# Performance work log

Hardware: AMD Instinct MI355X
Metric: run time of the kernel (lower is better)

Reference implementation:

```python
import jax, jax.numpy as jnp
import numpy as np
from jax import lax

NP = 27  # num_param, perfect cube
N3 = 3   # cube root
EPS = 1e-5


def _conv3d(x, w, stride, pad):
    return lax.conv_general_dilated(
        x, w, window_strides=(stride,) * 3, padding=[(pad, pad)] * 3,
        dimension_numbers=("NCDHW", "OIDHW", "NCDHW"))


def _p_n():
    # torch.meshgrid(arange(3),arange(3),arange(3), indexing='xy') == np.meshgrid 'xy'
    g0, g1, g2 = np.meshgrid(np.arange(N3), np.arange(N3), np.arange(N3), indexing="xy")
    p_n = np.concatenate([g0.ravel(), g1.ravel(), g2.ravel()], 0)  # (3N,)
    return jnp.asarray(p_n, jnp.float32).reshape(1, 3 * NP, 1, 1, 1)


def _p_0(h, w, d):
    # faithful to original: 'xy' meshgrid, flatten, then view(1,1,h,w,d)
    g0, g1, g2 = np.meshgrid(np.arange(h), np.arange(w), np.arange(d), indexing="xy")
    outs = []
    for g in (g0, g1, g2):
        gg = jnp.asarray(g.ravel(), jnp.float32).reshape(1, 1, h, w, d)
        outs.append(jnp.broadcast_to(gg, (1, NP, h, w, d)))
    return jnp.concatenate(outs, axis=1)  # (1, 3N, h, w, d)


def _gather_xq(x_flat, ix, iy, iz, W, D, shape):
    # x_flat: (b, c, H*W*D); i*: (b, h, w, d, N) int32
    idx = ix * (W * D) + iy * D + iz
    b = idx.shape[0]
    idx = jnp.clip(idx, 0, x_flat.shape[-1] - 1).reshape(b, -1)
    xq = jax.vmap(lambda xf, ii: xf[:, ii])(x_flat, idx)  # (b, c, h*w*d*N)
    return xq.reshape(shape)


def reference(x, p_w, p_b, conv_w, gamma, beta):
    b, c, H, W, D = x.shape
    # offset prediction (weight is zero-initialized in original; bias drives offsets)
    offset = _conv3d(x, p_w, 1, 1) + p_b[None, :, None, None, None]  # (b, 3N, h, w, d)
    h, w, d = offset.shape[2:]

    p = _p_0(h, w, d) + _p_n() + offset                 # (b, 3N, h, w, d)
    p = jnp.transpose(p, (0, 2, 3, 4, 1))               # (b, h, w, d, 3N)
    px, py, pz = p[..., :NP], p[..., NP:2 * NP], p[..., 2 * NP:]

    fx, fy, fz = jnp.floor(px), jnp.floor(py), jnp.floor(pz)
    ltx = jnp.clip(fx, 0, H - 1); lty = jnp.clip(fy, 0, W - 1); ltz = jnp.clip(fz, 0, D - 1)
    rbx = jnp.clip(fx + 1, 0, H - 1); rby = jnp.clip(fy + 1, 0, W - 1); rbz = jnp.clip(fz + 1, 0, D - 1)

    pcx = jnp.clip(px, 0, H - 1); pcy = jnp.clip(py, 0, W - 1); pcz = jnp.clip(pz, 0, D - 1)

    # trilinear-style weights (6 corners as in the original)
    g_lt = (1 + (ltx - pcx)) * (1 + (lty - pcy)) * (1 + (ltz - pcz))
    g_rb = (1 - (rbx - pcx)) * (1 - (rby - pcy)) * (1 - (rbz - pcz))
    g_lb = (1 + (ltx - pcx)) * (1 - (rby - pcy)) * (1 + (ltz - pcz))
    g_rt = (1 - (rbx - pcx)) * (1 + (lty - pcy)) * (1 + (ltz - pcz))
    g_lf = (1 + (ltx - pcx)) * (1 + (lty - pcy)) * (1 - (rbz - pcz))
    g_rf = (1 - (rbx - pcx)) * (1 - (rby - pcy)) * (1 + (ltz - pcz))

    i = lambda t: t.astype(jnp.int32)
    x_flat = x.reshape(b, c, -1)
    shp = (b, c, h, w, d, NP)
    xq_lt = _gather_xq(x_flat, i(ltx), i(lty), i(ltz), W, D, shp)
    xq_rb = _gather_xq(x_flat, i(rbx), i(rby), i(rbz), W, D, shp)
    xq_lb = _gather_xq(x_flat, i(ltx), i(rby), i(ltz), W, D, shp)
    xq_rt = _gather_xq(x_flat, i(rbx), i(lty), i(ltz), W, D, shp)
    xq_lf = _gather_xq(x_flat, i(ltx), i(lty), i(rbz), W, D, shp)
    xq_rf = _gather_xq(x_flat, i(rbx), i(rby), i(ltz), W, D, shp)

    e = lambda g: g[:, None]  # (b,1,h,w,d,N)
    x_off = (e(g_lt) * xq_lt + e(g_rb) * xq_rb + e(g_lb) * xq_lb +
             e(g_rt) * xq_rt + e(g_lf) * xq_lf + e(g_rf) * xq_rf)

    # regroup (b,c,h,w,d,27) -> (b,c,3h,3w,3d)
    x_off = x_off.reshape(b, c, h, w, d, N3, N3, N3)
    x_off = jnp.transpose(x_off, (0, 1, 2, 5, 3, 6, 4, 7)).reshape(b, c, h * N3, w * N3, d * N3)

    # Conv3d(stride 2, pad 1, no bias) + BatchNorm3d (train mode, batch stats) + SiLU
    o = _conv3d(x_off, conv_w, 2, 1)
    mean = jnp.mean(o, axis=(0, 2, 3, 4), keepdims=True)
    var = jnp.var(o, axis=(0, 2, 3, 4), keepdims=True)
    y = gamma[None, :, None, None, None] * (o - mean) * lax.rsqrt(var + EPS) + beta[None, :, None, None, None]
    return y * jax.nn.sigmoid(y)


def setup_inputs() -> dict:
    key = jax.random.key(0)
    k1, k2, k3 = jax.random.split(key, 3)
    B, Cin, Cout, S = 2, 16, 32, 32
    x = jax.random.normal(k1, (B, Cin, S, S, S), jnp.float32)
    p_w = jnp.zeros((3 * NP, Cin, 3, 3, 3), jnp.float32)  # zero-init as in original
    bound = 1.0 / np.sqrt(Cin * 27)
    p_b = jax.random.uniform(k2, (3 * NP,), jnp.float32, -bound, bound)
    conv_w = jax.random.normal(k3, (Cout, Cin, 3, 3, 3), jnp.float32) * 0.05
    gamma = jnp.ones((Cout,), jnp.float32)
    beta = jnp.zeros((Cout,), jnp.float32)
    return {"x": x, "p_w": p_w, "p_b": p_b, "conv_w": conv_w, "gamma": gamma, "beta": beta}
```

## Files before the change

### kernel.cpp

```cpp
#include <hip/hip_runtime.h>
#include <hip/hip_bf16.h>

constexpr int BATCH = 2;
constexpr int CIN   = 16;
constexpr int COUT  = 32;
constexpr int HWD   = 32768;
constexpr int BIG   = 96;
constexpr int OUTD  = 48;
constexpr int OUT2  = OUTD * OUTD;
constexpr int OUTN  = OUTD * OUTD * OUTD;
constexpr int NOUT  = BATCH * COUT * OUTN;
constexpr int NBLK3 = 1728;

typedef __attribute__((ext_vector_type(2)))  float f32x2;
typedef __attribute__((ext_vector_type(8)))  short bf16x8;
typedef __attribute__((ext_vector_type(16))) float f32x16;

__device__ __forceinline__ float bf_lo(uint u) { return __uint_as_float(u << 16); }
__device__ __forceinline__ float bf_hi(uint u) { return __uint_as_float(u & 0xFFFF0000u); }
__device__ __forceinline__ f32x2 up2(uint u) {
    f32x2 r; r.x = bf_lo(u); r.y = bf_hi(u); return r;
}

__global__ __launch_bounds__(256) void k_prep(const float* __restrict__ cw,
                                              const float* __restrict__ pw,
                                              const float* __restrict__ x,
                                              ushort* __restrict__ wTb,
                                              ushort* __restrict__ pwTb,
                                              ushort* __restrict__ xb,
                                              uint* __restrict__ lut) {
    int blk = blockIdx.x;
    if (blk < 216) {
        int t = blk * 256 + threadIdx.x;
        if (t < 13824) {
            int ci = t & 15; int rr = t >> 4; int co = rr & 31; int tap = rr >> 5;
            __hip_bfloat16 h = __float2bfloat16(cw[co * 432 + ci * 27 + tap]);
            wTb[t] = *(ushort*)&h;
        } else {
            int u = t - 13824;
            int ci = u & 15; int rr = u >> 4; int oc = rr % 96; int tap = rr / 96;
            float v = (oc < 81) ? pw[oc * 432 + ci * 27 + tap] : 0.f;
            __hip_bfloat16 h = __float2bfloat16(v);
            pwTb[u] = *(ushort*)&h;
        }
    } else if (blk < 222) {
        int e = (blk - 216) * 256 + threadIdx.x;
        if (e < 1445) {
            int su = e / 289; int rm = e - su * 289;
            int sv = rm / 17; int ts = rm - sv * 17;
            int sw = (ts < 9) ? (2 * ts) : (2 * ts - 17);
            lut[e] = (uint)su | ((uint)sv << 8) | ((uint)sw << 16) | ((uint)ts << 24);
        }
    } else {
        int t = (blk - 222) * 256 + threadIdx.x;
        int bt = t >> 15, pos = t & 32767;
        float v[16];
#pragma unroll
        for (int ci = 0; ci < 16; ci++) v[ci] = x[(bt * 16 + ci) * HWD + pos];
        uint uw[8];
#pragma unroll
        for (int cc = 0; cc < 8; cc++) {
            __hip_bfloat16 h0 = __float2bfloat16(v[2 * cc]);
            __hip_bfloat16 h1 = __float2bfloat16(v[2 * cc + 1]);
            uw[cc] = (uint)(*(ushort*)&h0) | ((uint)(*(ushort*)&h1) << 16);
        }
        uint4* xd = (uint4*)(xb + (size_t)t * 16);
        xd[0] = make_uint4(uw[0], uw[1], uw[2], uw[3]);
        xd[1] = make_uint4(uw[4], uw[5], uw[6], uw[7]);
    }
}

__global__ __launch_bounds__(256) void k_offset_mfma(const ushort* __restrict__ xb,
                                                     const ushort* __restrict__ pwTb,
                                                     const float* __restrict__ p_b,
                                                     ushort* __restrict__ offP) {
    __shared__ uint4 repbuf[1728];
    uint4*  lds = repbuf;
    ushort* rep = (ushort*)repbuf;

    int blk = blockIdx.x;
    int bt = blk >> 8; int r = blk & 255;
    int ut = r >> 4; int vt = (r >> 2) & 3; int wt = r & 3;
    int a0 = ut * 2, b0 = vt * 8, c0 = wt * 8;
    int tid = threadIdx.x;
    int wv = tid >> 6, l = tid & 63, col = l & 31, half = l >> 5;

    const ushort* xbb = xb + (size_t)bt * HWD * 16;
    for (int s = tid; s < 800; s += 256) {
        int h = s & 1, p = s >> 1;
        int su = p / 100; int rm = p - su * 100;
        int sv = rm / 10; int sw = rm - sv * 10;
        int ga = a0 - 1 + su, gb = b0 - 1 + sv, gc = c0 - 1 + sw;
        uint4 v = make_uint4(0, 0, 0, 0);
        if ((unsigned)ga < 32u && (unsigned)gb < 32u && (unsigned)gc < 32u)
            v = *(const uint4*)(xbb + (size_t)(ga * 1024 + gb * 32 + gc) * 16 + h * 8);
        lds[((su * 10 + sv) * 11 + sw) * 2 + h] = v;
    }
    __syncthreads();

    int U = wv >> 1, V = ((wv & 1) << 2) + (col >> 3), W = col & 7;
    const uint4* wt4 = (const uint4*)pwTb;

    f32x16 acc[3];
#pragma unroll 1
    for (int g = 0; g < 3; g++) {
        bf16x8 wf[27];
#pragma unroll
        for (int t = 0; t < 27; t++)
            wf[t] = __builtin_bit_cast(bf16x8, wt4[(t * 96 + g * 32 + col) * 2 + half]);
#pragma unroll
        for (int i = 0; i < 16; i++) acc[g][i] = 0.f;
#pragma unroll
        for (int k1 = 0; k1 < 3; k1++)
#pragma unroll
        for (int k2 = 0; k2 < 3; k2++)
#pragma unroll
        for (int k3 = 0; k3 < 3; k3++) {
            bf16x8 xf = __builtin_bit_cast(bf16x8,
                lds[(((U + k1) * 10 + (V + k2)) * 11 + (W + k3)) * 2 + half]);
            acc[g] = __builtin_amdgcn_mfma_f32_32x32x16_bf16(wf[(k1 * 3 + k2) * 3 + k3],
                                                             xf, acc[g], 0, 0, 0);
        }
    }
    __syncthreads();

    int posl = (U * 8 + V) * 8 + W;
#pragma unroll 1
    for (int g = 0; g < 3; g++) {
#pragma unroll
        for (int rg = 0; rg < 16; rg++) {
            int co = g * 32 + (rg & 3) + 8 * (rg >> 2) + 4 * half;
            if (co < 81) {
                int n = co % 27, d = co / 27;
                __hip_bfloat16 h = __float2bfloat16(acc[g][rg] + p_b[co]);
                rep[posl * 108 + n * 4 + d] = *(ushort*)&h;
            }
        }
    }
    __syncthreads();

    const uint* rp = (const uint*)rep;
    uint* og = (uint*)offP + (size_t)bt * HWD * 54;
    for (int f = tid; f < 6912; f += 256) {
        int pl = f / 54; int i = f - pl * 54;
        int pu = pl >> 6, pv = (pl >> 3) & 7, pw2 = pl & 7;
        int pos = (a0 + pu) * 1024 + (b0 + pv) * 32 + (c0 + pw2);
        og[(size_t)pos * 54 + i] = rp[f];
    }
}

__global__ __launch_bounds__(256, 3) void k_fused(const ushort* __restrict__ xb,
                                                  const ushort* __restrict__ offP,
                                                  const ushort* __restrict__ wTb,
                                                  const uint* __restrict__ lut,
                                                  ushort* __restrict__ o16,
                                                  float* __restrict__ psum,
                                                  float* __restrict__ psq) {
    __shared__ uint4 halo[5 * 17 * 19 * 2];
    __shared__ float ls[4][32], lq[4][32];

    int blk = (blockIdx.x & 7) * 216 + (blockIdx.x >> 3);

    int bt = blk / 864; int r = blk - bt * 864;
    int ut = r / 36; r -= ut * 36;
    int vt = r / 6;  int wt = r - vt * 6;

    int tid = threadIdx.x;
    int wv = tid >> 6, l = tid & 63;
    int col = l & 31, half = l >> 5;

    int gU0 = ut * 4 - 1, gV0 = vt * 16 - 1, gW0 = wt * 16 - 1;
    const ushort* xbb  = xb + (size_t)bt * HWD * 16;
    const ushort* offb = offP + (size_t)bt * HWD * 108;

    for (int s = tid; s < 1445; s += 256) {
        uint code = lut[s];
        int su = code & 255, sv = (code >> 8) & 255;
        int sw = (code >> 16) & 255, ts = code >> 24;
        int gU = gU0 + su, gV = gV0 + sv, gW = gW0 + sw;
        float vf = ((gU | gV | gW) >= 0) ? 1.f : 0.f;
        unsigned uU = (unsigned)max(gU, 0);
        unsigned uV = (unsigned)max(gV, 0);
        unsigned uW = (unsigned)max(gW, 0);
        int a = uU / 3u, i = uU - 3u * a;
        int b = uV / 3u, j = uV - 3u * b;
        int c = uW / 3u, kk = uW - 3u * c;
        int n = i * 9 + j * 3 + kk;
        int pos = a * 1024 + b * 32 + c;
        uint2 ou = *(const uint2*)(offb + (size_t)pos * 108 + n * 4);
        float ox = bf_lo(ou.x), oy = bf_hi(ou.x), oz = bf_lo(ou.y);

        float px = (float)(b + j) + ox;
        float py = (float)(a + i) + oy;
        float pz = (float)(c + kk) + oz;

        float fx = floorf(px), fy = floorf(py), fz = floorf(pz);
        float ltx = fminf(fmaxf(fx, 0.f), 31.f);
        float lty = fminf(fmaxf(fy, 0.f), 31.f);
        float ltz = fminf(fmaxf(fz, 0.f), 31.f);
        float rbx = fminf(fmaxf(fx + 1.f, 0.f), 31.f);
        float rby = fminf(fmaxf(fy + 1.f, 0.f), 31.f);
        float rbz = fminf(fmaxf(fz + 1.f, 0.f), 31.f);
        float pcx = fminf(fmaxf(px, 0.f), 31.f);
        float pcy = fminf(fmaxf(py, 0.f), 31.f);
        float pcz = fminf(fmaxf(pz, 0.f), 31.f);

        float axl = (1.f + (ltx - pcx)) * vf, axr = (1.f - (rbx - pcx)) * vf;
        float ayl = 1.f + (lty - pcy), ayr = 1.f - (rby - pcy);
        float azl = 1.f + (ltz - pcz), azr = 1.f - (rbz - pcz);

        float g_lt = axl * ayl * azl;
        float g_rb = axr * ayr * azr;
        float g_lb = axl * ayr * azl;
        float g_rt = axr * ayl * azl;
        float g_lf = axl * ayl * azr;
        float g_rf = axr * ayr * azl;

        int iltx = (int)ltx, ilty = (int)lty, iltz = (int)ltz;
        int irbx = (int)rbx, irby = (int)rby, irbz = (int)rbz;

        int i_lt = iltx * 1024 + ilty * 32 + iltz;
        int i_rb = irbx * 1024 + irby * 32 + irbz;
        int i_lb = iltx * 1024 + irby * 32 + iltz;
        int i_rt = irbx * 1024 + ilty * 32 + iltz;
        int i_lf = iltx * 1024 + ilty * 32 + irbz;
        int i_rf = irbx * 1024 + irby * 32 + iltz;

        f32x2 acc2[8];
#pragma unroll
        for (int q = 0; q < 8; q++) acc2[q] = (f32x2){0.f, 0.f};

        auto corner = [&](float g, int ip) {
            const uint4* p = (const uint4*)(xbb + (size_t)ip * 16);
            uint4 u0 = p[0], u1 = p[1];
            f32x2 g2 = {g, g};
            acc2[0] += g2 * up2(u0.x); acc2[1] += g2 * up2(u0.y);
            acc2[2] += g2 * up2(u0.z); acc2[3] += g2 * up2(u0.w);
            acc2[4] += g2 * up2(u1.x); acc2[5] += g2 * up2(u1.y);
            acc2[6] += g2 * up2(u1.z); acc2[7] += g2 * up2(u1.w);
        };
        corner(g_lt, i_lt);
        corner(g_rb, i_rb);
        corner(g_lb, i_lb);
        corner(g_rt, i_rt);
        corner(g_lf, i_lf);
        corner(g_rf, i_rf);

        uint uw[8];
#pragma unroll
        for (int cc = 0; cc < 8; cc++) {
            __hip_bfloat16 h0 = __float2bfloat16(acc2[cc].x);
            __hip_bfloat16 h1 = __float2bfloat16(acc2[cc].y);
            uw[cc] = (uint)(*(ushort*)&h0) | ((uint)(*(ushort*)&h1) << 16);
        }
        halo[((su * 17 + sv) * 19 + ts) * 2 + 0] = make_uint4(uw[0], uw[1], uw[2], uw[3]);
        halo[((su * 17 + sv) * 19 + ts) * 2 + 1] = make_uint4(uw[4], uw[5], uw[6], uw[7]);
    }

    bf16x8 wf[27];
    const uint4* wt4 = (const uint4*)wTb;
#pragma unroll
    for (int t = 0; t < 27; t++)
        wf[t] = __builtin_bit_cast(bf16x8, wt4[(t * 32 + col) * 2 + half]);

    __syncthreads();

    int U = wv >> 1, V = (wv & 1) * 4 + (col >> 3), W = col & 7;
    const uint4* lp = &halo[(((2 * U * 17 + 2 * V) * 19) + W) * 2 + half];

    f32x16 acc;
#pragma unroll
    for (int i = 0; i < 16; i++) acc[i] = 0.f;

#pragma unroll
    for (int k1 = 0; k1 < 3; k1++)
#pragma unroll
    for (int k2 = 0; k2 < 3; k2++)
#pragma unroll
    for (int k3 = 0; k3 < 3; k3++) {
        const int so = (k3 == 0) ? 0 : (k3 == 1 ? 9 : 1);
        const int off2 = ((k1 * 17 + k2) * 19 + so) * 2;
        bf16x8 xf = __builtin_bit_cast(bf16x8, lp[off2]);
        acc = __builtin_amdgcn_mfma_f32_32x32x16_bf16(wf[(k1 * 3 + k2) * 3 + k3],
                                                      xf, acc, 0, 0, 0);
    }

    int u = ut * 2 + U, v = vt * 8 + V, wg = wt * 8 + W;
    size_t posg = (size_t)u * OUT2 + v * OUTD + wg;
    ushort* ob = o16 + (size_t)bt * COUT * OUTN;
#pragma unroll
    for (int rg = 0; rg < 16; rg++) {
        int co = (rg & 3) + 8 * (rg >> 2) + 4 * half;
        __hip_bfloat16 h = __float2bfloat16(acc[rg]);
        ob[(size_t)co * OUTN + posg] = *(ushort*)&h;
    }

#pragma unroll
    for (int rg = 0; rg < 16; rg++) {
        float s = acc[rg], q = acc[rg] * acc[rg];
#pragma unroll
        for (int o = 1; o < 32; o <<= 1) {
            s += __shfl_xor(s, o);
            q += __shfl_xor(q, o);
        }
        if (col == 0) {
            int co = (rg & 3) + 8 * (rg >> 2) + 4 * half;
            ls[wv][co] = s; lq[wv][co] = q;
        }
    }
    __syncthreads();
    if (tid < 32) {
        float s = ls[0][tid] + ls[1][tid] + ls[2][tid] + ls[3][tid];
        float q = lq[0][tid] + lq[1][tid] + lq[2][tid] + lq[3][tid];
        psum[blk * 32 + tid] = s;
        psq[blk * 32 + tid]  = q;
    }
}

__global__ __launch_bounds__(256) void k_stats(const float* __restrict__ psum,
                                               const float* __restrict__ psq,
                                               const float* __restrict__ gamma,
                                               const float* __restrict__ beta,
                                               float* __restrict__ stats) {
    int co  = blockIdx.x;
    int tid = threadIdx.x;
    float s = 0.f, q = 0.f;
    for (int i = tid; i < NBLK3; i += 256) {
        s += psum[i * 32 + co];
        q += psq[i * 32 + co];
    }
    __shared__ float ss[256], sq[256];
    ss[tid] = s; sq[tid] = q;
    __syncthreads();
    for (int st = 128; st > 0; st >>= 1) {
        if (tid < st) { ss[tid] += ss[tid + st]; sq[tid] += sq[tid + st]; }
        __syncthreads();
    }
    if (tid == 0) {
        const float N = 221184.f;
        float mean = ss[0] / N;
        float var  = sq[0] / N - mean * mean;
        float inv  = rsqrtf(var + 1e-5f);
        float A = gamma[co] * inv;
        stats[co * 2]     = A;
        stats[co * 2 + 1] = beta[co] - A * mean;
    }
}

__global__ __launch_bounds__(256) void k_bn_silu(const ushort* __restrict__ o16,
                                                 const float* __restrict__ stats,
                                                 float* __restrict__ out) {
    int t = blockIdx.x * 256 + threadIdx.x;
    int co = (t / (OUTN / 8)) & 31;
    float A = stats[co * 2], B = stats[co * 2 + 1];
    uint4 u = ((const uint4*)o16)[t];
    float o[8] = {bf_lo(u.x), bf_hi(u.x), bf_lo(u.y), bf_hi(u.y),
                  bf_lo(u.z), bf_hi(u.z), bf_lo(u.w), bf_hi(u.w)};
    float y[8];
#pragma unroll
    for (int q = 0; q < 8; q++) {
        float yy = A * o[q] + B;
        y[q] = yy / (1.f + __expf(-yy));
    }
    float4* dst = (float4*)(out + (size_t)t * 8);
    dst[0] = make_float4(y[0], y[1], y[2], y[3]);
    dst[1] = make_float4(y[4], y[5], y[6], y[7]);
}

extern "C" void kernel_launch(void* const* d_in, const int* in_sizes, int n_in,
                              void* d_out, int out_size, void* d_ws, size_t ws_size,
                              hipStream_t stream) {
    const float* x      = (const float*)d_in[0];
    const float* p_w    = (const float*)d_in[1];
    const float* p_b    = (const float*)d_in[2];
    const float* conv_w = (const float*)d_in[3];
    const float* gamma  = (const float*)d_in[4];
    const float* beta   = (const float*)d_in[5];
    float* out = (float*)d_out;
    float* ws  = (float*)d_ws;

    float* psum  = ws;
    float* psq   = psum + 55296;
    float* stats = psq + 55296;
    ushort* wTb  = (ushort*)(stats + 64);
    ushort* pwTb = wTb + 13824;
    ushort* xb   = pwTb + 41472;
    ushort* offP = xb + 1048576;
    ushort* o16  = offP + 7077888;
    uint*   lut  = (uint*)(o16 + 7077888);

    k_prep<<<478, 256, 0, stream>>>(conv_w, p_w, x, wTb, pwTb, xb, lut);
    k_offset_mfma<<<512, 256, 0, stream>>>(xb, pwTb, p_b, offP);
    k_fused<<<NBLK3, 256, 0, stream>>>(xb, offP, wTb, lut, o16, psum, psq);
    k_stats<<<32, 256, 0, stream>>>(psum, psq, gamma, beta, stats);
    k_bn_silu<<<NOUT / 2048, 256, 0, stream>>>(o16, stats, out);
}
```

Baseline: 107.0 us.

## Use 512-thread blocks for halo gather and keep MFMA on 256 threads

Doubles the k_fused block to 512 threads. All threads share the deformable trilinear gather that fills the shared-memory halo, in a fixed three-iteration unrolled loop. The LUT is padded with dummy entries, written to a spare halo column, so no bounds check is needed. The halo is split into separate low and high channel arrays, and only the first 256 threads load weights and run the MFMA convolution and stats reduction. This aims to hide gather latency with more waves, but leaves half the threads idle during the MFMA phase, and the tighter launch bounds may force register spills of the 27 weight fragments.

```diff
diff --git a/kernel.cpp b/kernel.cpp
--- a/kernel.cpp
+++ b/kernel.cpp
@@ -45,12 +45,15 @@
         }
     } else if (blk < 222) {
         int e = (blk - 216) * 256 + threadIdx.x;
+        uint su, sv, sw, ts;
         if (e < 1445) {
-            int su = e / 289; int rm = e - su * 289;
-            int sv = rm / 17; int ts = rm - sv * 17;
-            int sw = (ts < 9) ? (2 * ts) : (2 * ts - 17);
-            lut[e] = (uint)su | ((uint)sv << 8) | ((uint)sw << 16) | ((uint)ts << 24);
-        }
+            su = e / 289; int rm = e - su * 289;
+            sv = rm / 17; ts = rm - sv * 17;
+            sw = (ts < 9) ? (2 * ts) : (2 * ts - 17);
+        } else {
+            su = 0; sv = (e - 1445) % 17; sw = 0; ts = 17;
+        }
+        lut[e] = su | (sv << 8) | (sw << 16) | (ts << 24);
     } else {
         int t = (blk - 222) * 256 + threadIdx.x;
         int bt = t >> 15, pos = t & 32767;
@@ -149,14 +152,15 @@
     }
 }
 
-__global__ __launch_bounds__(256, 3) void k_fused(const ushort* __restrict__ xb,
+__global__ __launch_bounds__(512, 6) void k_fused(const ushort* __restrict__ xb,
                                                   const ushort* __restrict__ offP,
                                                   const ushort* __restrict__ wTb,
                                                   const uint* __restrict__ lut,
                                                   ushort* __restrict__ o16,
                                                   float* __restrict__ psum,
                                                   float* __restrict__ psq) {
-    __shared__ uint4 halo[5 * 17 * 19 * 2];
+    __shared__ uint4 halo_lo[5 * 17 * 19];
+    __shared__ uint4 halo_hi[5 * 17 * 19];
     __shared__ float ls[4][32], lq[4][32];
 
     int blk = (blockIdx.x & 7) * 216 + (blockIdx.x >> 3);
@@ -166,14 +170,14 @@
     int vt = r / 6;  int wt = r - vt * 6;
 
     int tid = threadIdx.x;
-    int wv = tid >> 6, l = tid & 63;
-    int col = l & 31, half = l >> 5;
 
     int gU0 = ut * 4 - 1, gV0 = vt * 16 - 1, gW0 = wt * 16 - 1;
     const ushort* xbb  = xb + (size_t)bt * HWD * 16;
     const ushort* offb = offP + (size_t)bt * HWD * 108;
 
-    for (int s = tid; s < 1445; s += 256) {
+#pragma unroll
+    for (int it = 0; it < 3; it++) {
+        int s = tid + it * 512;
         uint code = lut[s];
         int su = code & 255, sv = (code >> 8) & 255;
         int sw = (code >> 16) & 255, ts = code >> 24;
@@ -253,59 +257,65 @@
             __hip_bfloat16 h1 = __float2bfloat16(acc2[cc].y);
             uw[cc] = (uint)(*(ushort*)&h0) | ((uint)(*(ushort*)&h1) << 16);
         }
-        halo[((su * 17 + sv) * 19 + ts) * 2 + 0] = make_uint4(uw[0], uw[1], uw[2], uw[3]);
-        halo[((su * 17 + sv) * 19 + ts) * 2 + 1] = make_uint4(uw[4], uw[5], uw[6], uw[7]);
-    }
-
-    bf16x8 wf[27];
-    const uint4* wt4 = (const uint4*)wTb;
-#pragma unroll
-    for (int t = 0; t < 27; t++)
-        wf[t] = __builtin_bit_cast(bf16x8, wt4[(t * 32 + col) * 2 + half]);
-
-    __syncthreads();
-
-    int U = wv >> 1, V = (wv & 1) * 4 + (col >> 3), W = col & 7;
-    const uint4* lp = &halo[(((2 * U * 17 + 2 * V) * 19) + W) * 2 + half];
-
-    f32x16 acc;
-#pragma unroll
-    for (int i = 0; i < 16; i++) acc[i] = 0.f;
-
-#pragma unroll
-    for (int k1 = 0; k1 < 3; k1++)
-#pragma unroll
-    for (int k2 = 0; k2 < 3; k2++)
-#pragma unroll
-    for (int k3 = 0; k3 < 3; k3++) {
-        const int so = (k3 == 0) ? 0 : (k3 == 1 ? 9 : 1);
-        const int off2 = ((k1 * 17 + k2) * 19 + so) * 2;
-        bf16x8 xf = __builtin_bit_cast(bf16x8, lp[off2]);
-        acc = __builtin_amdgcn_mfma_f32_32x32x16_bf16(wf[(k1 * 3 + k2) * 3 + k3],
-                                                      xf, acc, 0, 0, 0);
-    }
-
-    int u = ut * 2 + U, v = vt * 8 + V, wg = wt * 8 + W;
-    size_t posg = (size_t)u * OUT2 + v * OUTD + wg;
-    ushort* ob = o16 + (size_t)bt * COUT * OUTN;
-#pragma unroll
-    for (int rg = 0; rg < 16; rg++) {
-        int co = (rg & 3) + 8 * (rg >> 2) + 4 * half;
-        __hip_bfloat16 h = __float2bfloat16(acc[rg]);
-        ob[(size_t)co * OUTN + posg] = *(ushort*)&h;
-    }
-
-#pragma unroll
-    for (int rg = 0; rg < 16; rg++) {
-        float s = acc[rg], q = acc[rg] * acc[rg];
-#pragma unroll
-        for (int o = 1; o < 32; o <<= 1) {
-            s += __shfl_xor(s, o);
-            q += __shfl_xor(q, o);
-        }
-        if (col == 0) {
+        int idx = (su * 17 + sv) * 19 + ts;
+        halo_lo[idx] = make_uint4(uw[0], uw[1], uw[2], uw[3]);
+        halo_hi[idx] = make_uint4(uw[4], uw[5], uw[6], uw[7]);
+    }
+
+    __syncthreads();
+
+    if (tid < 256) {
+        int wv = tid >> 6, l = tid & 63;
+        int col = l & 31, half = l >> 5;
+
+        bf16x8 wf[27];
+        const uint4* wt4 = (const uint4*)wTb;
+#pragma unroll
+        for (int t = 0; t < 27; t++)
+            wf[t] = __builtin_bit_cast(bf16x8, wt4[(t * 32 + col) * 2 + half]);
+
+        int U = wv >> 1, V = (wv & 1) * 4 + (col >> 3), W = col & 7;
+        const uint4* base = half ? halo_hi : halo_lo;
+        const uint4* lp = &base[(2 * U * 17 + 2 * V) * 19 + W];
+
+        f32x16 acc;
+#pragma unroll
+        for (int i = 0; i < 16; i++) acc[i] = 0.f;
+
+#pragma unroll
+        for (int k1 = 0; k1 < 3; k1++)
+#pragma unroll
+        for (int k2 = 0; k2 < 3; k2++)
+#pragma unroll
+        for (int k3 = 0; k3 < 3; k3++) {
+            const int so = (k3 == 0) ? 0 : (k3 == 1 ? 9 : 1);
+            bf16x8 xf = __builtin_bit_cast(bf16x8, lp[(k1 * 17 + k2) * 19 + so]);
+            acc = __builtin_amdgcn_mfma_f32_32x32x16_bf16(wf[(k1 * 3 + k2) * 3 + k3],
+                                                          xf, acc, 0, 0, 0);
+        }
+
+        int u = ut * 2 + U, v = vt * 8 + V, wg = wt * 8 + W;
+        size_t posg = (size_t)u * OUT2 + v * OUTD + wg;
+        ushort* ob = o16 + (size_t)bt * COUT * OUTN;
+#pragma unroll
+        for (int rg = 0; rg < 16; rg++) {
             int co = (rg & 3) + 8 * (rg >> 2) + 4 * half;
-            ls[wv][co] = s; lq[wv][co] = q;
+            __hip_bfloat16 h = __float2bfloat16(acc[rg]);
+            ob[(size_t)co * OUTN + posg] = *(ushort*)&h;
+        }
+
+#pragma unroll
+        for (int rg = 0; rg < 16; rg++) {
+            float s = acc[rg], q = acc[rg] * acc[rg];
+#pragma unroll
+            for (int o = 1; o < 32; o <<= 1) {
+                s += __shfl_xor(s, o);
+                q += __shfl_xor(q, o);
+            }
+            if (col == 0) {
+                int co = (rg & 3) + 8 * (rg >> 2) + 4 * half;
+                ls[wv][co] = s; lq[wv][co] = q;
+            }
         }
     }
     __syncthreads();
@@ -391,7 +401,7 @@
 
     k_prep<<<478, 256, 0, stream>>>(conv_w, p_w, x, wTb, pwTb, xb, lut);
     k_offset_mfma<<<512, 256, 0, stream>>>(xb, pwTb, p_b, offP);
-    k_fused<<<NBLK3, 256, 0, stream>>>(xb, offP, wTb, lut, o16, psum, psq);
+    k_fused<<<NBLK3, 512, 0, stream>>>(xb, offP, wTb, lut, o16, psum, psq);
     k_stats<<<32, 256, 0, stream>>>(psum, psq, gamma, beta, stats);
     k_bn_silu<<<NOUT / 2048, 256, 0, stream>>>(o16, stats, out);
 }
```

Measured after the change: 105.5 us. About the same (-1.4%).

## Split halo gather across thread pairs and software-pipeline corner loads

Applied to the files above, without the earlier changes.

The fused deformable-gather+conv kernel now runs 512 threads per block, with each pair of threads gathering one halo sample (each thread handles 8 of the 16 channels). The halo build is unrolled into six iterations using a three-stage rotating buffer, so the gather loads for one sample are issued before the previous sample is blended. The halo-coordinate LUT is removed and its values are recomputed inline. Only the first 256 threads run the MFMA conv. The goal is more memory-level parallelism and latency hiding in the gather. The cost is higher register pressure under launch bounds of 512 threads with a minimum of 4 blocks per CU, plus idle threads during the MFMA phase.

```diff
diff --git a/kernel.cpp b/kernel.cpp
--- a/kernel.cpp
+++ b/kernel.cpp
@@ -27,8 +27,7 @@
                                               const float* __restrict__ x,
                                               ushort* __restrict__ wTb,
                                               ushort* __restrict__ pwTb,
-                                              ushort* __restrict__ xb,
-                                              uint* __restrict__ lut) {
+                                              ushort* __restrict__ xb) {
     int blk = blockIdx.x;
     if (blk < 216) {
         int t = blk * 256 + threadIdx.x;
@@ -43,16 +42,8 @@
             __hip_bfloat16 h = __float2bfloat16(v);
             pwTb[u] = *(ushort*)&h;
         }
-    } else if (blk < 222) {
-        int e = (blk - 216) * 256 + threadIdx.x;
-        if (e < 1445) {
-            int su = e / 289; int rm = e - su * 289;
-            int sv = rm / 17; int ts = rm - sv * 17;
-            int sw = (ts < 9) ? (2 * ts) : (2 * ts - 17);
-            lut[e] = (uint)su | ((uint)sv << 8) | ((uint)sw << 16) | ((uint)ts << 24);
-        }
     } else {
-        int t = (blk - 222) * 256 + threadIdx.x;
+        int t = (blk - 216) * 256 + threadIdx.x;
         int bt = t >> 15, pos = t & 32767;
         float v[16];
 #pragma unroll
@@ -149,14 +140,14 @@
     }
 }
 
-__global__ __launch_bounds__(256, 3) void k_fused(const ushort* __restrict__ xb,
+__global__ __launch_bounds__(512, 4) void k_fused(const ushort* __restrict__ xb,
                                                   const ushort* __restrict__ offP,
                                                   const ushort* __restrict__ wTb,
-                                                  const uint* __restrict__ lut,
                                                   ushort* __restrict__ o16,
                                                   float* __restrict__ psum,
                                                   float* __restrict__ psq) {
-    __shared__ uint4 halo[5 * 17 * 19 * 2];
+    __shared__ uint4 halo_lo[5 * 17 * 19];
+    __shared__ uint4 halo_hi[5 * 17 * 19];
     __shared__ float ls[4][32], lq[4][32];
 
     int blk = (blockIdx.x & 7) * 216 + (blockIdx.x >> 3);
@@ -166,25 +157,28 @@
     int vt = r / 6;  int wt = r - vt * 6;
 
     int tid = threadIdx.x;
-    int wv = tid >> 6, l = tid & 63;
-    int col = l & 31, half = l >> 5;
 
     int gU0 = ut * 4 - 1, gV0 = vt * 16 - 1, gW0 = wt * 16 - 1;
     const ushort* xbb  = xb + (size_t)bt * HWD * 16;
     const ushort* offb = offP + (size_t)bt * HWD * 108;
 
-    for (int s = tid; s < 1445; s += 256) {
-        uint code = lut[s];
-        int su = code & 255, sv = (code >> 8) & 255;
-        int sw = (code >> 16) & 255, ts = code >> 24;
+    int sbase = tid >> 1, half = tid & 1;
+    const ushort* xh = xbb + half * 8;
+    uint4* hb = half ? halo_hi : halo_lo;
+
+    auto PREP = [&](int it, int* ix, float* g, int& dsi) {
+        int s = it * 256 + sbase;
+        int su = (unsigned)s / 289u; int rm = s - su * 289;
+        int sv = (unsigned)rm / 17u; int ts = rm - sv * 17;
+        int sw = (ts < 9) ? (2 * ts) : (2 * ts - 17);
+        if (s >= 1445) { su = 0; sv = s & 15; ts = 17; sw = 0; }
+        dsi = (su * 17 + sv) * 19 + ts;
         int gU = gU0 + su, gV = gV0 + sv, gW = gW0 + sw;
         float vf = ((gU | gV | gW) >= 0) ? 1.f : 0.f;
-        unsigned uU = (unsigned)max(gU, 0);
-        unsigned uV = (unsigned)max(gV, 0);
-        unsigned uW = (unsigned)max(gW, 0);
-        int a = uU / 3u, i = uU - 3u * a;
-        int b = uV / 3u, j = uV - 3u * b;
-        int c = uW / 3u, kk = uW - 3u * c;
+        int uU = gU < 0 ? 0 : gU, uV = gV < 0 ? 0 : gV, uW = gW < 0 ? 0 : gW;
+        int a = (unsigned)uU / 3u, i = uU - 3 * a;
+        int b = (unsigned)uV / 3u, j = uV - 3 * b;
+        int c = (unsigned)uW / 3u, kk = uW - 3 * c;
         int n = i * 9 + j * 3 + kk;
         int pos = a * 1024 + b * 32 + c;
         uint2 ou = *(const uint2*)(offb + (size_t)pos * 108 + n * 4);
@@ -209,103 +203,117 @@
         float ayl = 1.f + (lty - pcy), ayr = 1.f - (rby - pcy);
         float azl = 1.f + (ltz - pcz), azr = 1.f - (rbz - pcz);
 
-        float g_lt = axl * ayl * azl;
-        float g_rb = axr * ayr * azr;
-        float g_lb = axl * ayr * azl;
-        float g_rt = axr * ayl * azl;
-        float g_lf = axl * ayl * azr;
-        float g_rf = axr * ayr * azl;
+        g[0] = axl * ayl * azl;
+        g[1] = axr * ayr * azr;
+        g[2] = axl * ayr * azl;
+        g[3] = axr * ayl * azl;
+        g[4] = axl * ayl * azr;
+        g[5] = axr * ayr * azl;
 
         int iltx = (int)ltx, ilty = (int)lty, iltz = (int)ltz;
         int irbx = (int)rbx, irby = (int)rby, irbz = (int)rbz;
 
-        int i_lt = iltx * 1024 + ilty * 32 + iltz;
-        int i_rb = irbx * 1024 + irby * 32 + irbz;
-        int i_lb = iltx * 1024 + irby * 32 + iltz;
-        int i_rt = irbx * 1024 + ilty * 32 + iltz;
-        int i_lf = iltx * 1024 + ilty * 32 + irbz;
-        int i_rf = irbx * 1024 + irby * 32 + iltz;
-
-        f32x2 acc2[8];
-#pragma unroll
-        for (int q = 0; q < 8; q++) acc2[q] = (f32x2){0.f, 0.f};
-
-        auto corner = [&](float g, int ip) {
-            const uint4* p = (const uint4*)(xbb + (size_t)ip * 16);
-            uint4 u0 = p[0], u1 = p[1];
-            f32x2 g2 = {g, g};
-            acc2[0] += g2 * up2(u0.x); acc2[1] += g2 * up2(u0.y);
-            acc2[2] += g2 * up2(u0.z); acc2[3] += g2 * up2(u0.w);
-            acc2[4] += g2 * up2(u1.x); acc2[5] += g2 * up2(u1.y);
-            acc2[6] += g2 * up2(u1.z); acc2[7] += g2 * up2(u1.w);
+        ix[0] = iltx * 1024 + ilty * 32 + iltz;
+        ix[1] = irbx * 1024 + irby * 32 + irbz;
+        ix[2] = iltx * 1024 + irby * 32 + iltz;
+        ix[3] = irbx * 1024 + ilty * 32 + iltz;
+        ix[4] = iltx * 1024 + ilty * 32 + irbz;
+        ix[5] = irbx * 1024 + irby * 32 + iltz;
+    };
+    auto ISSUE = [&](const int* ix, uint4* f) {
+#pragma unroll
+        for (int k = 0; k < 6; k++)
+            f[k] = *(const uint4*)(xh + (size_t)ix[k] * 16);
+    };
+    auto FIN = [&](const float* g, const uint4* f, int dsi) {
+        f32x2 a0 = {0.f, 0.f}, a1 = a0, a2 = a0, a3 = a0;
+#pragma unroll
+        for (int k = 0; k < 6; k++) {
+            f32x2 g2 = {g[k], g[k]};
+            a0 += g2 * up2(f[k].x);
+            a1 += g2 * up2(f[k].y);
+            a2 += g2 * up2(f[k].z);
+            a3 += g2 * up2(f[k].w);
+        }
+        auto pk = [](f32x2 v) -> uint {
+            __hip_bfloat16 h0 = __float2bfloat16(v.x);
+            __hip_bfloat16 h1 = __float2bfloat16(v.y);
+            return (uint)(*(ushort*)&h0) | ((uint)(*(ushort*)&h1) << 16);
         };
-        corner(g_lt, i_lt);
-        corner(g_rb, i_rb);
-        corner(g_lb, i_lb);
-        corner(g_rt, i_rt);
-        corner(g_lf, i_lf);
-        corner(g_rf, i_rf);
-
-        uint uw[8];
-#pragma unroll
-        for (int cc = 0; cc < 8; cc++) {
-            __hip_bfloat16 h0 = __float2bfloat16(acc2[cc].x);
-            __hip_bfloat16 h1 = __float2bfloat16(acc2[cc].y);
-            uw[cc] = (uint)(*(ushort*)&h0) | ((uint)(*(ushort*)&h1) << 16);
-        }
-        halo[((su * 17 + sv) * 19 + ts) * 2 + 0] = make_uint4(uw[0], uw[1], uw[2], uw[3]);
-        halo[((su * 17 + sv) * 19 + ts) * 2 + 1] = make_uint4(uw[4], uw[5], uw[6], uw[7]);
-    }
-
-    bf16x8 wf[27];
-    const uint4* wt4 = (const uint4*)wTb;
-#pragma unroll
-    for (int t = 0; t < 27; t++)
-        wf[t] = __builtin_bit_cast(bf16x8, wt4[(t * 32 + col) * 2 + half]);
-
-    __syncthreads();
-
-    int U = wv >> 1, V = (wv & 1) * 4 + (col >> 3), W = col & 7;
-    const uint4* lp = &halo[(((2 * U * 17 + 2 * V) * 19) + W) * 2 + half];
-
-    f32x16 acc;
-#pragma unroll
-    for (int i = 0; i < 16; i++) acc[i] = 0.f;
-
-#pragma unroll
-    for (int k1 = 0; k1 < 3; k1++)
-#pragma unroll
-    for (int k2 = 0; k2 < 3; k2++)
-#pragma unroll
-    for (int k3 = 0; k3 < 3; k3++) {
-        const int so = (k3 == 0) ? 0 : (k3 == 1 ? 9 : 1);
-        const int off2 = ((k1 * 17 + k2) * 19 + so) * 2;
-        bf16x8 xf = __builtin_bit_cast(bf16x8, lp[off2]);
-        acc = __builtin_amdgcn_mfma_f32_32x32x16_bf16(wf[(k1 * 3 + k2) * 3 + k3],
-                                                      xf, acc, 0, 0, 0);
-    }
-
-    int u = ut * 2 + U, v = vt * 8 + V, wg = wt * 8 + W;
-    size_t posg = (size_t)u * OUT2 + v * OUTD + wg;
-    ushort* ob = o16 + (size_t)bt * COUT * OUTN;
-#pragma unroll
-    for (int rg = 0; rg < 16; rg++) {
-        int co = (rg & 3) + 8 * (rg >> 2) + 4 * half;
-        __hip_bfloat16 h = __float2bfloat16(acc[rg]);
-        ob[(size_t)co * OUTN + posg] = *(ushort*)&h;
-    }
-
-#pragma unroll
-    for (int rg = 0; rg < 16; rg++) {
-        float s = acc[rg], q = acc[rg] * acc[rg];
-#pragma unroll
-        for (int o = 1; o < 32; o <<= 1) {
-            s += __shfl_xor(s, o);
-            q += __shfl_xor(q, o);
-        }
-        if (col == 0) {
-            int co = (rg & 3) + 8 * (rg >> 2) + 4 * half;
-            ls[wv][co] = s; lq[wv][co] = q;
+        hb[dsi] = make_uint4(pk(a0), pk(a1), pk(a2), pk(a3));
+    };
+
+    int   ixA[6], ixB[6], ixC[6], dsA, dsB, dsC;
+    float gA[6], gB[6], gC[6];
+    uint4 fA[6], fB[6], fC[6];
+
+    PREP(0, ixA, gA, dsA); ISSUE(ixA, fA);
+    PREP(1, ixB, gB, dsB); ISSUE(ixB, fB);
+    FIN(gA, fA, dsA);
+    PREP(2, ixC, gC, dsC); ISSUE(ixC, fC);
+    FIN(gB, fB, dsB);
+    PREP(3, ixA, gA, dsA); ISSUE(ixA, fA);
+    FIN(gC, fC, dsC);
+    PREP(4, ixB, gB, dsB); ISSUE(ixB, fB);
+    FIN(gA, fA, dsA);
+    PREP(5, ixC, gC, dsC); ISSUE(ixC, fC);
+    FIN(gB, fB, dsB);
+    FIN(gC, fC, dsC);
+
+    __syncthreads();
+
+    if (tid < 256) {
+        int wv = tid >> 6, l = tid & 63;
+        int col = l & 31, mh = l >> 5;
+
+        bf16x8 wf[27];
+        const uint4* wt4 = (const uint4*)wTb;
+#pragma unroll
+        for (int t = 0; t < 27; t++)
+            wf[t] = __builtin_bit_cast(bf16x8, wt4[(t * 32 + col) * 2 + mh]);
+
+        int U = wv >> 1, V = (wv & 1) * 4 + (col >> 3), W = col & 7;
+        const uint4* base = mh ? halo_hi : halo_lo;
+        const uint4* lp = &base[(2 * U * 17 + 2 * V) * 19 + W];
+
+        f32x16 acc;
+#pragma unroll
+        for (int i = 0; i < 16; i++) acc[i] = 0.f;
+
+#pragma unroll
+        for (int k1 = 0; k1 < 3; k1++)
+#pragma unroll
+        for (int k2 = 0; k2 < 3; k2++)
+#pragma unroll
+        for (int k3 = 0; k3 < 3; k3++) {
+            const int so = (k3 == 0) ? 0 : (k3 == 1 ? 9 : 1);
+            bf16x8 xf = __builtin_bit_cast(bf16x8, lp[(k1 * 17 + k2) * 19 + so]);
+            acc = __builtin_amdgcn_mfma_f32_32x32x16_bf16(wf[(k1 * 3 + k2) * 3 + k3],
+                                                          xf, acc, 0, 0, 0);
+        }
+
+        int u = ut * 2 + U, v = vt * 8 + V, wg = wt * 8 + W;
+        size_t posg = (size_t)u * OUT2 + v * OUTD + wg;
+        ushort* ob = o16 + (size_t)bt * COUT * OUTN;
+#pragma unroll
+        for (int rg = 0; rg < 16; rg++) {
+            int co = (rg & 3) + 8 * (rg >> 2) + 4 * mh;
+            __hip_bfloat16 h = __float2bfloat16(acc[rg]);
+            ob[(size_t)co * OUTN + posg] = *(ushort*)&h;
+        }
+
+#pragma unroll
+        for (int rg = 0; rg < 16; rg++) {
+            float s = acc[rg], q = acc[rg] * acc[rg];
+#pragma unroll
+            for (int o = 1; o < 32; o <<= 1) {
+                s += __shfl_xor(s, o);
+                q += __shfl_xor(q, o);
+            }
+            if (col == 0) {
+                int co = (rg & 3) + 8 * (rg >> 2) + 4 * mh;
+                ls[wv][co] = s; lq[wv][co] = q;
+            }
         }
     }
     __syncthreads();
@@ -387,11 +395,10 @@
     ushort* xb   = pwTb + 41472;
     ushort* offP = xb + 1048576;
     ushort* o16  = offP + 7077888;
-    uint*   lut  = (uint*)(o16 + 7077888);
-
-    k_prep<<<478, 256, 0, stream>>>(conv_w, p_w, x, wTb, pwTb, xb, lut);
+
+    k_prep<<<472, 256, 0, stream>>>(conv_w, p_w, x, wTb, pwTb, xb);
     k_offset_mfma<<<512, 256, 0, stream>>>(xb, pwTb, p_b, offP);
-    k_fused<<<NBLK3, 256, 0, stream>>>(xb, offP, wTb, lut, o16, psum, psq);
+    k_fused<<<NBLK3, 512, 0, stream>>>(xb, offP, wTb, o16, psum, psq);
     k_stats<<<32, 256, 0, stream>>>(psum, psq, gamma, beta, stats);
     k_bn_silu<<<NOUT / 2048, 256, 0, stream>>>(o16, stats, out);
 }
```

Result: faster. 104.1 us (-2.8%).
